# Kernel tuning notes

Measured on AMD Instinct MI355X. Metric: run time of the kernel, lower is better.

Reference implementation:

```python
import jax, jax.numpy as jnp
import numpy as np

# config
B, V, S, D = 2, 8, 256, 2048
NH, NKV, KVR = 32, 8, 2
HD = D // NH            # 64
G = NH // NKV           # GQA group size = 4
INIT = 0.02


def _neighbor_idx():
    # replicates generate_neighbor: left neighbors (i-half..i-1) then right (i+1..i+half), circular
    half = KVR // 2
    offsets = np.concatenate([np.arange(-half, 0), np.arange(1, half + 1)])
    return (np.arange(V)[:, None] + offsets[None, :]) % V  # [V, KVR]


def setup_inputs() -> dict:
    key = jax.random.key(0)
    k1, k2, k3, k4 = jax.random.split(key, 4)
    x = jax.random.normal(k1, (B, V, S, D), jnp.float32)
    wq = jax.random.normal(k2, (D, NH * HD), jnp.float32) * INIT
    wkv = jax.random.normal(k3, (D, 2 * NKV * HD), jnp.float32) * INIT
    wo = jax.random.normal(k4, (D, D), jnp.float32) * INIT
    return {"x": x, "wq": wq, "wkv": wkv, "wo": wo}


def reference(x, wq, wkv, wo):
    b, v, s, d = x.shape
    idx = _neighbor_idx()  # [V, KVR] static

    # Q projection: [b, v, s, NH*HD]
    xq = (x @ wq).reshape(b, v, s, NKV, G, HD)  # grouped-query layout (kv head, group)

    # neighbor gather: [b, v, KVR, s, d] -> [b, v, KVR*s, d]
    x_kv = x[:, idx].reshape(b, v, KVR * s, d)
    kv = x_kv @ wkv
    xk, xv = jnp.split(kv, 2, axis=-1)
    xk = xk.reshape(b, v, KVR * s, NKV, HD)
    xv = xv.reshape(b, v, KVR * s, NKV, HD)

    # grouped-query SDPA (no mask, eval mode): avoids materializing repeated K/V
    scale = 1.0 / jnp.sqrt(jnp.asarray(HD, x.dtype))
    scores = jnp.einsum('bvsngh,bvtnh->bvngst', xq, xk) * scale  # [b,v,NKV,G,s,KVR*s]
    attn = jax.nn.softmax(scores, axis=-1)
    out = jnp.einsum('bvngst,bvtnh->bvsngh', attn, xv).reshape(b, v, s, d)
    return out @ wo
```

## Files before the change

### kernel.cpp

```cpp
#include <hip/hip_runtime.h>
#include <stdint.h>

typedef unsigned short u16;
typedef unsigned int   u32;
typedef short short8 __attribute__((ext_vector_type(8)));
typedef float f32x4  __attribute__((ext_vector_type(4)));

__device__ __forceinline__ u16 f2bf(float f){
  u32 u = __builtin_bit_cast(u32, f);
  u32 r = (u + 0x7FFFu + ((u >> 16) & 1u)) >> 16;
  return (u16)r;
}
__device__ __forceinline__ u32 cvtpk(float a, float b){
  u32 r; asm("v_cvt_pk_bf16_f32 %0, %1, %2" : "=v"(r) : "v"(a), "v"(b)); return r;
}
__device__ __forceinline__ void gload16(const u16* g, u16* l){
  __builtin_amdgcn_global_load_lds((const __attribute__((address_space(1))) void*)g,
                                   (__attribute__((address_space(3))) void*)l, 16, 0, 0);
}
#define BARRIER()  do{ __builtin_amdgcn_s_barrier(); __builtin_amdgcn_sched_barrier(0); }while(0)

__device__ __forceinline__ void dev_transpose(const float* __restrict__ in,
                                              u16* __restrict__ out, int R, int C,
                                              int bid, int tx, int ty, float (*tile)[33]){
  int nc = C >> 5;
  int cb = bid % nc, rb = bid / nc;
#pragma unroll
  for (int i = 0; i < 4; ++i){
    int r = rb * 32 + ty + i * 8;
    tile[ty + i * 8][tx] = in[(size_t)r * C + cb * 32 + tx];
  }
  __syncthreads();
#pragma unroll
  for (int i = 0; i < 4; ++i){
    int c = cb * 32 + ty + i * 8;
    out[(size_t)c * R + rb * 32 + tx] = f2bf(tile[tx][ty + i * 8]);
  }
}

__global__ __launch_bounds__(256) void k_prep(const float* __restrict__ x,
                                              const float* __restrict__ wq,
                                              const float* __restrict__ wkv,
                                              const float* __restrict__ wo,
                                              u16* __restrict__ x_bf,
                                              u16* __restrict__ wqkvt,
                                              u16* __restrict__ wot){
  __shared__ float tile[32][33];
  int bid = blockIdx.x;
  if (bid < 4096){
    int i = bid * 256 + threadIdx.x;
    const float4* p = (const float4*)x + (size_t)i * 2;
    float4 a = p[0], b = p[1];
    short8 o;
    o[0] = f2bf(a.x); o[1] = f2bf(a.y); o[2] = f2bf(a.z); o[3] = f2bf(a.w);
    o[4] = f2bf(b.x); o[5] = f2bf(b.y); o[6] = f2bf(b.z); o[7] = f2bf(b.w);
    *(short8*)(x_bf + (size_t)i * 8) = o;
    return;
  }
  int tx = threadIdx.x & 31, ty = threadIdx.x >> 5;
  if (bid < 8192)       dev_transpose(wq,  wqkvt,               2048, 2048, bid - 4096,  tx, ty, tile);
  else if (bid < 10240) dev_transpose(wkv, wqkvt + 2048 * 2048, 2048, 1024, bid - 8192,  tx, ty, tile);
  else                  dev_transpose(wo,  wot,                 2048, 2048, bid - 10240, tx, ty, tile);
}

template<int BM, int BN, int MH, int NFRAG, int ALOADS, int BLOADS, bool QSCALE, typename CT>
__global__ __launch_bounds__(512) void k_gemm8p(const u16* __restrict__ A,
                                                const u16* __restrict__ Bt,
                                                CT* __restrict__ C,
                                                int N, int K){
  constexpr int SZA = BM * 128;
  constexpr int SZB = BN * 128;
  constexpr int SZ  = SZA + SZB;
  constexpr int WTM = BM / 2;
  constexpr int WTN = BN / 4;
  __shared__ char lds[2 * SZ];

  int tid = threadIdx.x, lane = tid & 63, wid = tid >> 6;
  int l16 = lane & 15, g4 = lane >> 4;
  int wm = wid >> 2, wn = wid & 3;
  int bid = blockIdx.x;
  int cpx = (int)gridDim.x >> 3;
  int wg = (bid & 7) * cpx + (bid >> 3);
  int nb = N / BN;
  int bm = wg / nb, bn = wg % nb;

  const u16* baseA = A  + (size_t)(bm * BM) * K;
  const u16* baseB = Bt + (size_t)(bn * BN) * K;

  int aLds[ALOADS], aG[ALOADS];
#pragma unroll
  for (int i = 0; i < ALOADS; ++i){
    int q = (wid * ALOADS + i) * 1024 + lane * 16;
    int row = q >> 7, c = q & 127;
    int cs = c ^ ((row & 7) << 4);
    aLds[i] = q; aG[i] = row * K + (cs >> 1);
  }
  int bLds[BLOADS], bG[BLOADS];
#pragma unroll
  for (int j = 0; j < BLOADS; ++j){
    int q = (wid * BLOADS + j) * 1024 + lane * 16;
    int row = q >> 7, c = q & 127;
    int cs = c ^ ((row & 7) << 4);
    bLds[j] = q; bG[j] = row * K + (cs >> 1);
  }
  auto stageA = [&](int t){
    char* dst = lds + (t & 1) * SZ;
#pragma unroll
    for (int i = 0; i < ALOADS; ++i) gload16(baseA + aG[i] + t * 64, (u16*)(dst + aLds[i]));
  };
  auto stageB = [&](int t){
    char* dst = lds + (t & 1) * SZ + SZA;
#pragma unroll
    for (int j = 0; j < BLOADS; ++j) gload16(baseB + bG[j] + t * 64, (u16*)(dst + bLds[j]));
  };
  auto rdA = [&](const char* Ab, int m, int ks){
    int row = wm * WTM + m * 16 + l16;
    return *(const short8*)(Ab + row * 128 + ((ks * 64 + g4 * 16) ^ ((row & 7) << 4)));
  };
  auto rdB = [&](const char* Bb, int nf, int ks){
    int row = wn * WTN + nf * 16 + l16;
    return *(const short8*)(Bb + row * 128 + ((ks * 64 + g4 * 16) ^ ((row & 7) << 4)));
  };

  f32x4 zero4 = {0.f, 0.f, 0.f, 0.f};
  f32x4 acc[2 * MH][NFRAG];
#pragma unroll
  for (int i = 0; i < 2 * MH; ++i)
#pragma unroll
    for (int j = 0; j < NFRAG; ++j) acc[i][j] = zero4;

  int NK = K >> 6;
  stageA(0); stageB(0);
  asm volatile("s_waitcnt vmcnt(0)" ::: "memory");
  BARRIER();
  short8 a0[MH], a1[MH], a2[MH], a3[MH], bf0[NFRAG], bf1[NFRAG];
#pragma unroll
  for (int nf = 0; nf < NFRAG; ++nf) bf0[nf] = rdB(lds + SZA, nf, 0);
#pragma unroll
  for (int m = 0; m < MH; ++m)       a0[m]  = rdA(lds, m, 0);

  for (int kt = 0; kt < NK; ++kt){
    const char* Ab = lds + (kt & 1) * SZ;
    const char* Bb = Ab + SZA;
    bool st = (kt + 1 < NK);
#pragma unroll
    for (int m = 0; m < MH; ++m) a1[m] = rdA(Ab, MH + m, 0);
    if (st) stageA(kt + 1);
    BARRIER();
    __builtin_amdgcn_s_setprio(1);
#pragma unroll
    for (int m = 0; m < MH; ++m)
#pragma unroll
      for (int nf = 0; nf < NFRAG; ++nf)
        acc[m][nf] = __builtin_amdgcn_mfma_f32_16x16x32_bf16(a0[m], bf0[nf], acc[m][nf], 0, 0, 0);
    __builtin_amdgcn_s_setprio(0);
#pragma unroll
    for (int nf = 0; nf < NFRAG; ++nf) bf1[nf] = rdB(Bb, nf, 1);
#pragma unroll
    for (int m = 0; m < MH; ++m)       a2[m]  = rdA(Ab, m, 1);
    if (st) stageB(kt + 1);
    BARRIER();
    __builtin_amdgcn_s_setprio(1);
#pragma unroll
    for (int m = 0; m < MH; ++m)
#pragma unroll
      for (int nf = 0; nf < NFRAG; ++nf)
        acc[MH + m][nf] = __builtin_amdgcn_mfma_f32_16x16x32_bf16(a1[m], bf0[nf], acc[MH + m][nf], 0, 0, 0);
    __builtin_amdgcn_s_setprio(0);
#pragma unroll
    for (int m = 0; m < MH; ++m) a3[m] = rdA(Ab, MH + m, 1);
    BARRIER();
    __builtin_amdgcn_s_setprio(1);
#pragma unroll
    for (int m = 0; m < MH; ++m)
#pragma unroll
      for (int nf = 0; nf < NFRAG; ++nf)
        acc[m][nf] = __builtin_amdgcn_mfma_f32_16x16x32_bf16(a2[m], bf1[nf], acc[m][nf], 0, 0, 0);
    __builtin_amdgcn_s_setprio(0);
    if (st) asm volatile("s_waitcnt vmcnt(0)" ::: "memory");
    BARRIER();
    if (st){
      const char* Ab2 = lds + ((kt + 1) & 1) * SZ;
      const char* Bb2 = Ab2 + SZA;
#pragma unroll
      for (int nf = 0; nf < NFRAG; ++nf) bf0[nf] = rdB(Bb2, nf, 0);
#pragma unroll
      for (int m = 0; m < MH; ++m)       a0[m]  = rdA(Ab2, m, 0);
    }
    __builtin_amdgcn_s_setprio(1);
#pragma unroll
    for (int m = 0; m < MH; ++m)
#pragma unroll
      for (int nf = 0; nf < NFRAG; ++nf)
        acc[MH + m][nf] = __builtin_amdgcn_mfma_f32_16x16x32_bf16(a3[m], bf1[nf], acc[MH + m][nf], 0, 0, 0);
    __builtin_amdgcn_s_setprio(0);
    BARRIER();
  }

#pragma unroll
  for (int mf = 0; mf < 2 * MH; ++mf)
#pragma unroll
    for (int nf = 0; nf < NFRAG; ++nf)
#pragma unroll
      for (int r = 0; r < 4; ++r){
        int row = bm * BM + wm * WTM + mf * 16 + g4 * 4 + r;
        int col = bn * BN + wn * WTN + nf * 16 + l16;
        float vv = acc[mf][nf][r];
        if constexpr (QSCALE) { if (col < 2048) vv *= 0.18033688011112042f; }
        if constexpr (sizeof(CT) == 2) C[(size_t)row * N + col] = (CT)f2bf(vv);
        else                           C[(size_t)row * N + col] = (CT)vv;
      }
}

__global__ __launch_bounds__(256) void k_vt(const u16* __restrict__ c1, u16* __restrict__ vt){
  __shared__ u16 tile[64][72];
  int bid = blockIdx.x;
  int st = bid & 3, n = (bid >> 2) & 7, bv = bid >> 5;
  int t = threadIdx.x;
  int sr = t >> 2, sc = t & 3;
  const u16* src = c1 + (size_t)(bv * 256 + st * 64 + sr) * 3072 + 2560 + n * 64 + sc * 16;
  short8 a = *(const short8*)src;
  short8 b = *(const short8*)(src + 8);
  *(short8*)&tile[sr][sc * 16]     = a;
  *(short8*)&tile[sr][sc * 16 + 8] = b;
  __syncthreads();
  int h = t >> 2, c2 = t & 3;
  short8 o0, o1;
#pragma unroll
  for (int j = 0; j < 8; ++j) o0[j] = (short)tile[c2 * 16 + j][h];
#pragma unroll
  for (int j = 0; j < 8; ++j) o1[j] = (short)tile[c2 * 16 + 8 + j][h];
  u16* dst = vt + (size_t)((bv * 8 + n) * 64 + h) * 256 + st * 64 + c2 * 16;
  *(short8*)dst       = o0;
  *(short8*)(dst + 8) = o1;
}

__global__ __launch_bounds__(256, 2) void k_attn(const u16* __restrict__ c1,
                                                 const u16* __restrict__ vt,
                                                 u16* __restrict__ att){
  __shared__ char KV[2][16384];
  __shared__ u16 Plds[4][16][72];
  int bid = blockIdx.x;
  int qt = bid & 3, n = (bid >> 2) & 7, v = (bid >> 5) & 7, b = bid >> 8;
  int tid = threadIdx.x;
  int g = tid >> 6, lane = tid & 63, l16 = lane & 15, g4 = lane >> 4;
  int bv = b * 8 + v;
  int rowQ = bv * 256 + qt * 64;
  int qcol = n * 256 + g * 64;

  int srow[2], scol[2], qo[2];
#pragma unroll
  for (int i = 0; i < 2; ++i){
    int q = i * 4096 + tid * 16;
    int row = q >> 7, c = q & 127;
    int cs = c ^ ((row & 7) << 4);
    srow[i] = row; scol[i] = cs >> 1; qo[i] = q;
  }
  auto stage = [&](int t, int buf){
    int vn = (t < 4) ? ((v + 7) & 7) : ((v + 1) & 7);
    int tb = (t & 3) * 64;
    const u16* kb = c1 + (size_t)((b * 8 + vn) * 256 + tb) * 3072 + 2048 + n * 64;
    const u16* vb = vt + (size_t)(((b * 8 + vn) * 8 + n) * 64) * 256 + tb;
    char* d = KV[buf];
#pragma unroll
    for (int i = 0; i < 2; ++i) gload16(kb + (size_t)srow[i] * 3072 + scol[i], (u16*)(d + qo[i]));
#pragma unroll
    for (int i = 0; i < 2; ++i) gload16(vb + (size_t)srow[i] * 256 + scol[i], (u16*)(d + 8192 + qo[i]));
  };
  auto rdK = [&](int buf, int kt, int ks){
    int row = kt * 16 + l16;
    return *(const short8*)(KV[buf] + row * 128 + ((ks * 64 + g4 * 16) ^ ((row & 7) << 4)));
  };
  auto rdV = [&](int buf, int hi, int ks){
    int row = hi * 16 + l16;
    return *(const short8*)(KV[buf] + 8192 + row * 128 + ((ks * 64 + g4 * 16) ^ ((row & 7) << 4)));
  };

  short8 qf[4][2];
#pragma unroll
  for (int qi = 0; qi < 4; ++qi)
#pragma unroll
    for (int kk = 0; kk < 2; ++kk)
      qf[qi][kk] = *(const short8*)(c1 + (size_t)(rowQ + qi * 16 + l16) * 3072
                                     + qcol + kk * 32 + g4 * 8);

  f32x4 zero4 = {0.f, 0.f, 0.f, 0.f};
  f32x4 O[4][4];
#pragma unroll
  for (int i = 0; i < 4; ++i)
#pragma unroll
    for (int j = 0; j < 4; ++j) O[i][j] = zero4;
  float m2[4]   = {-3.0e38f, -3.0e38f, -3.0e38f, -3.0e38f};
  float lsum[4] = {0.f, 0.f, 0.f, 0.f};

  stage(0, 0);
  __syncthreads();

  for (int ti = 0; ti < 8; ++ti){
    int buf = ti & 1;
    if (ti < 7) stage(ti + 1, buf ^ 1);
    short8 kf[4][2], vf[2][4];
#pragma unroll
    for (int kt = 0; kt < 4; ++kt)
#pragma unroll
      for (int ks = 0; ks < 2; ++ks)
        kf[kt][ks] = rdK(buf, kt, ks);
#pragma unroll
    for (int ks = 0; ks < 2; ++ks)
#pragma unroll
      for (int hi = 0; hi < 4; ++hi)
        vf[ks][hi] = rdV(buf, hi, ks);

#pragma unroll
    for (int qi = 0; qi < 4; ++qi){
      f32x4 sa[4];
#pragma unroll
      for (int kt = 0; kt < 4; ++kt){
        sa[kt] = zero4;
#pragma unroll
        for (int ks = 0; ks < 2; ++ks)
          sa[kt] = __builtin_amdgcn_mfma_f32_16x16x32_bf16(kf[kt][ks], qf[qi][ks], sa[kt], 0, 0, 0);
      }
      float pmax = sa[0][0];
#pragma unroll
      for (int kt = 0; kt < 4; ++kt)
#pragma unroll
        for (int r = 0; r < 4; ++r) pmax = fmaxf(pmax, sa[kt][r]);
      pmax = fmaxf(pmax, __shfl_xor(pmax, 16));
      pmax = fmaxf(pmax, __shfl_xor(pmax, 32));
      if (__any(pmax > m2[qi] + 8.f)){
        float mnew  = fmaxf(m2[qi], pmax);
        float alpha = exp2f(m2[qi] - mnew);
        m2[qi] = mnew;
        lsum[qi] *= alpha;
        float ab[4];
#pragma unroll
        for (int r = 0; r < 4; ++r) ab[r] = __shfl(alpha, g4 * 4 + r);
#pragma unroll
        for (int hi = 0; hi < 4; ++hi)
#pragma unroll
          for (int r = 0; r < 4; ++r) O[qi][hi][r] *= ab[r];
      }
      float m = m2[qi];
      float psum = 0.f;
      u32 w[4][2];
#pragma unroll
      for (int kt = 0; kt < 4; ++kt){
        float p0 = exp2f(sa[kt][0] - m);
        float p1 = exp2f(sa[kt][1] - m);
        float p2 = exp2f(sa[kt][2] - m);
        float p3 = exp2f(sa[kt][3] - m);
        psum += (p0 + p1) + (p2 + p3);
        w[kt][0] = cvtpk(p0, p1);
        w[kt][1] = cvtpk(p2, p3);
      }
      psum += __shfl_xor(psum, 16);
      psum += __shfl_xor(psum, 32);
      lsum[qi] += psum;
      u32* prow = (u32*)&Plds[g][l16][0];
#pragma unroll
      for (int kt = 0; kt < 4; ++kt){
        prow[kt * 8 + g4 * 2]     = w[kt][0];
        prow[kt * 8 + g4 * 2 + 1] = w[kt][1];
      }
      short8 pa[2];
#pragma unroll
      for (int ks = 0; ks < 2; ++ks)
        pa[ks] = *(const short8*)&Plds[g][l16][ks * 32 + g4 * 8];
#pragma unroll
      for (int hi = 0; hi < 4; ++hi)
#pragma unroll
        for (int ks = 0; ks < 2; ++ks)
          O[qi][hi] = __builtin_amdgcn_mfma_f32_16x16x32_bf16(pa[ks], vf[ks][hi], O[qi][hi], 0, 0, 0);
    }
    __syncthreads();
  }
#pragma unroll
  for (int qi = 0; qi < 4; ++qi){
    float lb[4];
#pragma unroll
    for (int r = 0; r < 4; ++r) lb[r] = 1.0f / __shfl(lsum[qi], g4 * 4 + r);
#pragma unroll
    for (int hi = 0; hi < 4; ++hi)
#pragma unroll
      for (int r = 0; r < 4; ++r){
        int row = rowQ + qi * 16 + g4 * 4 + r;
        int col = qcol + hi * 16 + l16;
        att[(size_t)row * 2048 + col] = f2bf(O[qi][hi][r] * lb[r]);
      }
  }
}

extern "C" void kernel_launch(void* const* d_in, const int* in_sizes, int n_in,
                              void* d_out, int out_size, void* d_ws, size_t ws_size,
                              hipStream_t stream){
  const float* x   = (const float*)d_in[0];
  const float* wq  = (const float*)d_in[1];
  const float* wkv = (const float*)d_in[2];
  const float* wo  = (const float*)d_in[3];
  float* out = (float*)d_out;
  char* ws = (char*)d_ws;

  u16* x_bf  = (u16*)(ws);
  u16* wqkvt = (u16*)(ws + 16777216);
  u16* wot   = (u16*)(ws + 29360128);
  u16* c1    = (u16*)(ws + 37748736);
  u16* vt    = (u16*)(ws + 62914560);
  u16* att   = x_bf;

  k_prep<<<14336, 256, 0, stream>>>(x, wq, wkv, wo, x_bf, wqkvt, wot);
  k_gemm8p<128, 192, 2, 3, 2, 3, true,  u16  ><<<512, 512, 0, stream>>>(x_bf, wqkvt, c1, 3072, 2048);
  k_vt<<<512, 256, 0, stream>>>(c1, vt);
  k_attn<<<512, 256, 0, stream>>>(c1, vt, att);
  k_gemm8p<128, 128, 2, 2, 2, 2, false, float><<<512, 512, 0, stream>>>(att, wot, out, 2048, 2048);
}
```

Baseline: 150.3 us.

## Switch GEMMs to 4-wave blocks with larger per-wave tiles

The GEMM kernel now runs 256 threads (4 waves) per block instead of 512 (8 waves). Each wave covers all BM rows and a quarter of the BN columns, so it holds a larger accumulator tile. The output projection also moves to a 128x256 tile with 256 blocks instead of 512. The aim is more MFMA work per LDS fragment read and fewer waves contending at barriers, at the cost of higher register pressure, fewer waves to hide latency, and a half-size grid for the second GEMM.

After: 161.0 us. 7.1% more time.

```diff
diff --git a/kernel.cpp b/kernel.cpp
--- a/kernel.cpp
+++ b/kernel.cpp
@@ -63,21 +63,21 @@
   else                  dev_transpose(wo,  wot,                 2048, 2048, bid - 10240, tx, ty, tile);
 }
 
-template<int BM, int BN, int MH, int NFRAG, int ALOADS, int BLOADS, bool QSCALE, typename CT>
-__global__ __launch_bounds__(512) void k_gemm8p(const u16* __restrict__ A,
+template<int BM, int BN, int NF, int ALOADS, int BLOADS, bool QSCALE, typename CT>
+__global__ __launch_bounds__(256) void k_gemm4n(const u16* __restrict__ A,
                                                 const u16* __restrict__ Bt,
                                                 CT* __restrict__ C,
                                                 int N, int K){
   constexpr int SZA = BM * 128;
   constexpr int SZB = BN * 128;
   constexpr int SZ  = SZA + SZB;
-  constexpr int WTM = BM / 2;
+  constexpr int MH  = BM / 32;
   constexpr int WTN = BN / 4;
   __shared__ char lds[2 * SZ];
 
   int tid = threadIdx.x, lane = tid & 63, wid = tid >> 6;
   int l16 = lane & 15, g4 = lane >> 4;
-  int wm = wid >> 2, wn = wid & 3;
+  int wn = wid;
   int bid = blockIdx.x;
   int cpx = (int)gridDim.x >> 3;
   int wg = (bid & 7) * cpx + (bid >> 3);
@@ -114,7 +114,7 @@
     for (int j = 0; j < BLOADS; ++j) gload16(baseB + bG[j] + t * 64, (u16*)(dst + bLds[j]));
   };
   auto rdA = [&](const char* Ab, int m, int ks){
-    int row = wm * WTM + m * 16 + l16;
+    int row = m * 16 + l16;
     return *(const short8*)(Ab + row * 128 + ((ks * 64 + g4 * 16) ^ ((row & 7) << 4)));
   };
   auto rdB = [&](const char* Bb, int nf, int ks){
@@ -123,21 +123,21 @@
   };
 
   f32x4 zero4 = {0.f, 0.f, 0.f, 0.f};
-  f32x4 acc[2 * MH][NFRAG];
+  f32x4 acc[2 * MH][NF];
 #pragma unroll
   for (int i = 0; i < 2 * MH; ++i)
 #pragma unroll
-    for (int j = 0; j < NFRAG; ++j) acc[i][j] = zero4;
+    for (int j = 0; j < NF; ++j) acc[i][j] = zero4;
 
   int NK = K >> 6;
   stageA(0); stageB(0);
   asm volatile("s_waitcnt vmcnt(0)" ::: "memory");
   BARRIER();
-  short8 a0[MH], a1[MH], a2[MH], a3[MH], bf0[NFRAG], bf1[NFRAG];
-#pragma unroll
-  for (int nf = 0; nf < NFRAG; ++nf) bf0[nf] = rdB(lds + SZA, nf, 0);
-#pragma unroll
-  for (int m = 0; m < MH; ++m)       a0[m]  = rdA(lds, m, 0);
+  short8 a0[MH], a1[MH], a2[MH], a3[MH], bf0[NF], bf1[NF];
+#pragma unroll
+  for (int nf = 0; nf < NF; ++nf) bf0[nf] = rdB(lds + SZA, nf, 0);
+#pragma unroll
+  for (int m = 0; m < MH; ++m)    a0[m]  = rdA(lds, m, 0);
 
   for (int kt = 0; kt < NK; ++kt){
     const char* Ab = lds + (kt & 1) * SZ;
@@ -151,20 +151,20 @@
 #pragma unroll
     for (int m = 0; m < MH; ++m)
 #pragma unroll
-      for (int nf = 0; nf < NFRAG; ++nf)
+      for (int nf = 0; nf < NF; ++nf)
         acc[m][nf] = __builtin_amdgcn_mfma_f32_16x16x32_bf16(a0[m], bf0[nf], acc[m][nf], 0, 0, 0);
     __builtin_amdgcn_s_setprio(0);
 #pragma unroll
-    for (int nf = 0; nf < NFRAG; ++nf) bf1[nf] = rdB(Bb, nf, 1);
-#pragma unroll
-    for (int m = 0; m < MH; ++m)       a2[m]  = rdA(Ab, m, 1);
+    for (int nf = 0; nf < NF; ++nf) bf1[nf] = rdB(Bb, nf, 1);
+#pragma unroll
+    for (int m = 0; m < MH; ++m)    a2[m]  = rdA(Ab, m, 1);
     if (st) stageB(kt + 1);
     BARRIER();
     __builtin_amdgcn_s_setprio(1);
 #pragma unroll
     for (int m = 0; m < MH; ++m)
 #pragma unroll
-      for (int nf = 0; nf < NFRAG; ++nf)
+      for (int nf = 0; nf < NF; ++nf)
         acc[MH + m][nf] = __builtin_amdgcn_mfma_f32_16x16x32_bf16(a1[m], bf0[nf], acc[MH + m][nf], 0, 0, 0);
     __builtin_amdgcn_s_setprio(0);
 #pragma unroll
@@ -174,7 +174,7 @@
 #pragma unroll
     for (int m = 0; m < MH; ++m)
 #pragma unroll
-      for (int nf = 0; nf < NFRAG; ++nf)
+      for (int nf = 0; nf < NF; ++nf)
         acc[m][nf] = __builtin_amdgcn_mfma_f32_16x16x32_bf16(a2[m], bf1[nf], acc[m][nf], 0, 0, 0);
     __builtin_amdgcn_s_setprio(0);
     if (st) asm volatile("s_waitcnt vmcnt(0)" ::: "memory");
@@ -183,15 +183,15 @@
       const char* Ab2 = lds + ((kt + 1) & 1) * SZ;
       const char* Bb2 = Ab2 + SZA;
 #pragma unroll
-      for (int nf = 0; nf < NFRAG; ++nf) bf0[nf] = rdB(Bb2, nf, 0);
-#pragma unroll
-      for (int m = 0; m < MH; ++m)       a0[m]  = rdA(Ab2, m, 0);
+      for (int nf = 0; nf < NF; ++nf) bf0[nf] = rdB(Bb2, nf, 0);
+#pragma unroll
+      for (int m = 0; m < MH; ++m)    a0[m]  = rdA(Ab2, m, 0);
     }
     __builtin_amdgcn_s_setprio(1);
 #pragma unroll
     for (int m = 0; m < MH; ++m)
 #pragma unroll
-      for (int nf = 0; nf < NFRAG; ++nf)
+      for (int nf = 0; nf < NF; ++nf)
         acc[MH + m][nf] = __builtin_amdgcn_mfma_f32_16x16x32_bf16(a3[m], bf1[nf], acc[MH + m][nf], 0, 0, 0);
     __builtin_amdgcn_s_setprio(0);
     BARRIER();
@@ -200,10 +200,10 @@
 #pragma unroll
   for (int mf = 0; mf < 2 * MH; ++mf)
 #pragma unroll
-    for (int nf = 0; nf < NFRAG; ++nf)
+    for (int nf = 0; nf < NF; ++nf)
 #pragma unroll
       for (int r = 0; r < 4; ++r){
-        int row = bm * BM + wm * WTM + mf * 16 + g4 * 4 + r;
+        int row = bm * BM + mf * 16 + g4 * 4 + r;
         int col = bn * BN + wn * WTN + nf * 16 + l16;
         float vv = acc[mf][nf][r];
         if constexpr (QSCALE) { if (col < 2048) vv *= 0.18033688011112042f; }
@@ -409,8 +409,8 @@
   u16* att   = x_bf;
 
   k_prep<<<14336, 256, 0, stream>>>(x, wq, wkv, wo, x_bf, wqkvt, wot);
-  k_gemm8p<128, 192, 2, 3, 2, 3, true,  u16  ><<<512, 512, 0, stream>>>(x_bf, wqkvt, c1, 3072, 2048);
+  k_gemm4n<128, 192, 3, 4, 6, true,  u16  ><<<512, 256, 0, stream>>>(x_bf, wqkvt, c1, 3072, 2048);
   k_vt<<<512, 256, 0, stream>>>(c1, vt);
   k_attn<<<512, 256, 0, stream>>>(c1, vt, att);
-  k_gemm8p<128, 128, 2, 2, 2, 2, false, float><<<512, 512, 0, stream>>>(att, wot, out, 2048, 2048);
-}
+  k_gemm4n<128, 256, 4, 4, 8, false, float><<<256, 256, 0, stream>>>(att, wot, out, 2048, 2048);
+}
```
